# Kernel optimization log

Hardware: AMD Instinct MI355X
Metric: run time of the kernel (lower is better)

## Reference

```python
import jax, jax.numpy as jnp
import numpy as np

B, N, E = 4, 10000, 160000
D, H, HID, DE = 128, 4, 128, 16
DK = HID // H


def setup_inputs() -> dict:
    key = jax.random.key(0)
    ks = jax.random.split(key, 16)
    w = lambda k, shape: jax.random.normal(k, shape, jnp.float32) * 0.02
    return {
        "x": jax.random.normal(ks[0], (B, N, D), jnp.float32),
        "edge_index": jax.random.randint(ks[1], (2, E), 0, N, dtype=jnp.int32),
        "edge_attr": jax.random.normal(ks[2], (E, DE), jnp.float32),
        "Wq": w(ks[3], (D, HID)), "bq": jnp.zeros((HID,), jnp.float32),
        "Wk": w(ks[4], (D, HID)), "bk": jnp.zeros((HID,), jnp.float32),
        "Wv": w(ks[5], (D, HID)), "bv": jnp.zeros((HID,), jnp.float32),
        "Wf": w(ks[6], (DE, 2 * HID)), "bf": jnp.zeros((2 * HID,), jnp.float32),
        "Wo": w(ks[7], (HID, D)), "bo": jnp.zeros((D,), jnp.float32),
        "ln_g": jnp.ones((D,), jnp.float32), "ln_b": jnp.zeros((D,), jnp.float32),
    }


def reference(x, edge_index, edge_attr, Wq, bq, Wk, bk, Wv, bv, Wf, bf, Wo, bo, ln_g, ln_b):
    src, dst = edge_index[0], edge_index[1]
    # node projections -> [B, N, H, DK]
    Q = (x @ Wq + bq).reshape(B, N, H, DK)
    K = (x @ Wk + bk).reshape(B, N, H, DK)
    V = (x @ Wv + bv).reshape(B, N, H, DK)
    # edge gathers -> [B, E, H, DK]
    q_e, k_e, v_e = Q[:, dst], K[:, src], V[:, src]
    # FiLM modulation of keys (edge-conditioned, shared across batch)
    gamma, beta = jnp.split(edge_attr @ Wf + bf, 2, axis=-1)
    gamma = gamma.reshape(1, E, H, DK)
    beta = beta.reshape(1, E, H, DK)
    k_e = k_e * (1.0 + gamma) + beta
    logits = (q_e * k_e).sum(-1) / np.sqrt(DK).astype(np.float32)  # [B, E, H]

    def seg_softmax(lg):  # lg: [E, H], softmax over edges sharing a dst node
        m = jax.ops.segment_max(lg, dst, num_segments=N)       # [N, H]
        ex = jnp.exp(lg - m[dst])
        s = jax.ops.segment_sum(ex, dst, num_segments=N)        # [N, H]
        return ex / s[dst]

    att = jax.vmap(seg_softmax)(logits)                         # [B, E, H]
    msg = att[..., None] * v_e                                  # [B, E, H, DK]
    agg = jax.vmap(lambda m: jax.ops.segment_sum(m, dst, num_segments=N))(msg)
    y = agg.reshape(B, N, HID) @ Wo + bo                        # [B, N, D]
    h = x + y  # dropout is identity in eval mode
    mu = h.mean(-1, keepdims=True)
    var = ((h - mu) ** 2).mean(-1, keepdims=True)
    return (h - mu) / jnp.sqrt(var + 1e-5) * ln_g + ln_b
```

## Files before the change

### kernel.cpp

```cpp
#include <hip/hip_runtime.h>
#include <hip/hip_bf16.h>

#define B_ 4
#define N_ 10000
#define E_ 160000
#define D_ 128
#define H_ 4
#define HID_ 128
#define DK_ 32
#define DE_ 16
#define PGRID 2048
#define QKV_BLKS 625
#define FILM_BLKS 512
#define HIST_BLKS 625

typedef __attribute__((ext_vector_type(8))) short short8v;
typedef __attribute__((ext_vector_type(4))) short short4v;
typedef __attribute__((ext_vector_type(4))) float f32x4;
typedef __attribute__((ext_vector_type(2))) float f32x2;

__device__ __forceinline__ short bfb(float f) {
  union { float f; unsigned u; } c; c.f = f;
  unsigned u = c.u + 0x7FFFu + ((c.u >> 16) & 1u);
  return (short)(u >> 16);
}
__device__ __forceinline__ float b2f(unsigned short u) {
  union { unsigned u; float f; } c; c.u = ((unsigned)u) << 16;
  return c.f;
}

__device__ __forceinline__ unsigned char f2fp8(float f) {
  int r = __builtin_amdgcn_cvt_pk_fp8_f32(f, f, 0, false);
  return (unsigned char)(r & 0xff);
}
__device__ __forceinline__ f32x2 fp8lo(unsigned u) {
  return __builtin_amdgcn_cvt_pk_f32_fp8((int)u, false);
}
__device__ __forceinline__ f32x2 fp8hi(unsigned u) {
  return __builtin_amdgcn_cvt_pk_f32_fp8((int)u, true);
}

__global__ __launch_bounds__(256) void wt_prep(
    const float* __restrict__ Wq, const float* __restrict__ Wk,
    const float* __restrict__ Wv, const float* __restrict__ Wo,
    short* __restrict__ wt) {
  const float* Ws[4] = {Wq, Wk, Wv, Wo};
  const int i = blockIdx.x * 256 + threadIdx.x;
  const int m = i >> 14;
  const int k = (i >> 7) & 127;
  const int n = i & 127;
  wt[(size_t)m * 16384 + n * 128 + k] = bfb(Ws[m][k * 128 + n]);
}

__global__ __launch_bounds__(256) void phase1(
    const float* __restrict__ x, const short* __restrict__ wt,
    const float* __restrict__ bq, const float* __restrict__ bk,
    const float* __restrict__ bv,
    unsigned short* __restrict__ Qb, unsigned char* __restrict__ kv8,
    const float* __restrict__ ea, const float* __restrict__ Wf,
    const float* __restrict__ bf, unsigned char* __restrict__ film8,
    const int* __restrict__ ei, int* __restrict__ cnt) {
  const int blk = blockIdx.x;

  if (blk < QKV_BLKS) {
    __shared__ short xs[4][16][136];
    const int wave = threadIdx.x >> 6;
    const int lane = threadIdx.x & 63;
    const int ln15 = lane & 15;
    const int g    = lane >> 4;
    const long rowBase = ((long)blk * 4 + wave) * 16;

    for (int i = lane; i < 16 * 32; i += 64) {
      const int r  = i >> 5;
      const int c4 = (i & 31) * 4;
      const float4 v = *(const float4*)(x + (rowBase + r) * 128 + c4);
      short4v sv; sv.x = bfb(v.x); sv.y = bfb(v.y); sv.z = bfb(v.z); sv.w = bfb(v.w);
      *(short4v*)&xs[wave][r][c4] = sv;
    }
    __syncthreads();

    short8v af[4];
#pragma unroll
    for (int kk = 0; kk < 4; ++kk)
      af[kk] = *(const short8v*)&xs[wave][ln15][kk * 32 + g * 8];

    const float* bs[3] = {bq, bk, bv};

    int bbv[4], nnv[4];
#pragma unroll
    for (int r = 0; r < 4; ++r) {
      const long row = rowBase + g * 4 + r;
      bbv[r] = (int)(row / N_);
      nnv[r] = (int)(row - (long)bbv[r] * N_);
    }

#pragma unroll
    for (int m = 0; m < 3; ++m) {
      const short* Wt = wt + (size_t)m * 16384;
      f32x4 acc[8];
#pragma unroll
      for (int cb = 0; cb < 8; ++cb) acc[cb] = (f32x4){0.f, 0.f, 0.f, 0.f};

#pragma unroll
      for (int kk = 0; kk < 4; ++kk) {
#pragma unroll
        for (int cb = 0; cb < 8; ++cb) {
          const short8v bfr =
              *(const short8v*)(Wt + (cb * 16 + ln15) * 128 + kk * 32 + g * 8);
          acc[cb] = __builtin_amdgcn_mfma_f32_16x16x32_bf16(af[kk], bfr, acc[cb], 0, 0, 0);
        }
      }

      const float* bias = bs[m];
#pragma unroll
      for (int cb = 0; cb < 8; ++cb) {
        const int col = cb * 16 + ln15;
        const float bv_ = bias[col];
#pragma unroll
        for (int r = 0; r < 4; ++r) {
          const float val = acc[cb][r] + bv_;
          if (m == 0) {
            const long row = rowBase + g * 4 + r;
            Qb[row * 128 + col] = (unsigned short)bfb(val);
          } else {
            kv8[(((size_t)nnv[r] * 4 + bbv[r]) << 8) + (m - 1) * 128 + col] = f2fp8(val);
          }
        }
      }
    }
  } else if (blk < QKV_BLKS + FILM_BLKS) {
    const int fb   = blk - QKV_BLKS;
    const int lane = threadIdx.x & 63;
    const int wave = threadIdx.x >> 6;
    const int c0 = lane * 4;

    float4 w[16];
#pragma unroll
    for (int j = 0; j < 16; ++j) w[j] = *(const float4*)(Wf + j * 256 + c0);
    const float4 bias = *(const float4*)(bf + c0);

    for (int i = fb * 4 + wave; i < E_; i += FILM_BLKS * 4) {
      const float* ep = ea + (size_t)i * 16;
      const float4 a0 = *(const float4*)ep;
      const float4 a1 = *(const float4*)(ep + 4);
      const float4 a2 = *(const float4*)(ep + 8);
      const float4 a3 = *(const float4*)(ep + 12);
      const float ev[16] = {a0.x,a0.y,a0.z,a0.w, a1.x,a1.y,a1.z,a1.w,
                            a2.x,a2.y,a2.z,a2.w, a3.x,a3.y,a3.z,a3.w};
      float ox = bias.x, oy = bias.y, oz = bias.z, ow = bias.w;
#pragma unroll
      for (int j = 0; j < 16; ++j) {
        ox = fmaf(ev[j], w[j].x, ox);
        oy = fmaf(ev[j], w[j].y, oy);
        oz = fmaf(ev[j], w[j].z, oz);
        ow = fmaf(ev[j], w[j].w, ow);
      }
      int r = __builtin_amdgcn_cvt_pk_fp8_f32(ox, oy, 0, false);
      r = __builtin_amdgcn_cvt_pk_fp8_f32(oz, ow, r, true);
      ((int*)(film8 + (size_t)i * 256))[lane] = r;
    }
  } else {
    const int e = (blk - QKV_BLKS - FILM_BLKS) * 256 + threadIdx.x;
    if (e < E_) atomicAdd(&cnt[ei[E_ + e]], 1);
  }
}

__global__ __launch_bounds__(1024) void csr_scan(const int* __restrict__ cnt,
                                                 int* __restrict__ rowptr,
                                                 int* __restrict__ fill) {
  __shared__ int part[1024];
  const int t = threadIdx.x;
  int local[10];
  int sum = 0;
#pragma unroll
  for (int i = 0; i < 10; ++i) {
    const int idx = t * 10 + i;
    local[i] = sum;
    sum += (idx < N_) ? cnt[idx] : 0;
  }
  part[t] = sum;
  __syncthreads();
  for (int off = 1; off < 1024; off <<= 1) {
    const int v = (t >= off) ? part[t - off] : 0;
    __syncthreads();
    part[t] += v;
    __syncthreads();
  }
  const int excl = (t == 0) ? 0 : part[t - 1];
#pragma unroll
  for (int i = 0; i < 10; ++i) {
    const int idx = t * 10 + i;
    if (idx <= N_) {
      const int o = excl + local[i];
      rowptr[idx] = o;
      if (idx < N_) fill[idx] = o;
    }
  }
}

__global__ __launch_bounds__(256) void csr_scatter(
    const int* __restrict__ ei, int* __restrict__ fill,
    int* __restrict__ esrc, int* __restrict__ eord) {
  const int e = blockIdx.x * 256 + threadIdx.x;
  if (e < E_) {
    const int dst = ei[E_ + e];
    const int pos = atomicAdd(&fill[dst], 1);
    esrc[pos] = ei[e];
    eord[pos] = e;
  }
}

__global__ __launch_bounds__(256) void fused_attn(
    const int* __restrict__ rowptr, const int* __restrict__ esrc,
    const int* __restrict__ eord, const unsigned char* __restrict__ film8,
    const unsigned short* __restrict__ Qb,
    const unsigned char* __restrict__ kv8, float* __restrict__ agg) {
  const int wave = threadIdx.x >> 6;
  const int lane = threadIdx.x & 63;
  const int e2 = lane >> 5;
  const int dh = (lane >> 4) & 1;
  const int b  = (lane >> 2) & 3;
  const int h  = lane & 3;
  const int col0 = h * 32 + dh * 16;

  for (int node = blockIdx.x * 4 + wave; node < N_; node += PGRID * 4) {
    const int beg = rowptr[node], end = rowptr[node + 1];

    float q[16];
    {
      const unsigned short* qp = Qb + ((size_t)b * N_ + node) * 128 + col0;
      const short8v t0 = *(const short8v*)qp;
      const short8v t1 = *(const short8v*)(qp + 8);
#pragma unroll
      for (int j = 0; j < 8; ++j) {
        q[j]     = b2f((unsigned short)t0[j]);
        q[8 + j] = b2f((unsigned short)t1[j]);
      }
    }
    float acc[16];
#pragma unroll
    for (int d = 0; d < 16; ++d) acc[d] = 0.f;
    float se = 0.f;

    for (int i0 = beg; i0 < end; i0 += 2) {
      const int ii = i0 + e2;
      const bool valid = ii < end;
      const int ic = valid ? ii : i0;
      const int src = esrc[ic];
      const int de  = eord[ic];
      const unsigned char* kp = kv8 + ((((size_t)src << 2) + b) << 8) + col0;
      const unsigned char* fp = film8 + (size_t)de * 256 + col0;
      const uint4 kw = *(const uint4*)kp;
      const uint4 vw = *(const uint4*)(kp + 128);
      const uint4 gw = *(const uint4*)fp;
      const uint4 tw = *(const uint4*)(fp + 128);
      const unsigned ks[4] = {kw.x, kw.y, kw.z, kw.w};
      const unsigned vs[4] = {vw.x, vw.y, vw.z, vw.w};
      const unsigned gs[4] = {gw.x, gw.y, gw.z, gw.w};
      const unsigned ts[4] = {tw.x, tw.y, tw.z, tw.w};

      float pacc[4] = {0.f, 0.f, 0.f, 0.f};
#pragma unroll
      for (int w = 0; w < 4; ++w) {
        const f32x2 k0 = fp8lo(ks[w]), k1 = fp8hi(ks[w]);
        const f32x2 g0 = fp8lo(gs[w]), g1 = fp8hi(gs[w]);
        const f32x2 t0 = fp8lo(ts[w]), t1 = fp8hi(ts[w]);
        float km;
        km = k0.x + fmaf(k0.x, g0.x, t0.x); pacc[w] = fmaf(q[4*w+0], km, pacc[w]);
        km = k0.y + fmaf(k0.y, g0.y, t0.y); pacc[w] = fmaf(q[4*w+1], km, pacc[w]);
        km = k1.x + fmaf(k1.x, g1.x, t1.x); pacc[w] = fmaf(q[4*w+2], km, pacc[w]);
        km = k1.y + fmaf(k1.y, g1.y, t1.y); pacc[w] = fmaf(q[4*w+3], km, pacc[w]);
      }
      float pl = (pacc[0] + pacc[1]) + (pacc[2] + pacc[3]);
      pl += __shfl_xor(pl, 16);

      float ex = __expf(pl * 0.17677669529663687f);
      ex = valid ? ex : 0.f;
      se += ex;
#pragma unroll
      for (int w = 0; w < 4; ++w) {
        const f32x2 v0 = fp8lo(vs[w]), v1 = fp8hi(vs[w]);
        acc[4*w+0] = fmaf(ex, v0.x, acc[4*w+0]);
        acc[4*w+1] = fmaf(ex, v0.y, acc[4*w+1]);
        acc[4*w+2] = fmaf(ex, v1.x, acc[4*w+2]);
        acc[4*w+3] = fmaf(ex, v1.y, acc[4*w+3]);
      }
    }

#pragma unroll
    for (int d = 0; d < 16; ++d) acc[d] += __shfl_xor(acc[d], 32);
    se += __shfl_xor(se, 32);

    if (e2 == 0) {
      const float inv = (end > beg) ? 1.f / se : 0.f;
      float* ap = agg + ((size_t)b * N_ + node) * 128 + col0;
#pragma unroll
      for (int c = 0; c < 4; ++c) {
        float4 o;
        o.x = acc[c*4+0] * inv; o.y = acc[c*4+1] * inv;
        o.z = acc[c*4+2] * inv; o.w = acc[c*4+3] * inv;
        *(float4*)(ap + c * 4) = o;
      }
    }
  }
}

__global__ __launch_bounds__(64) void out_ln_mfma(
    const float* __restrict__ agg, const short* __restrict__ wto,
    const float* __restrict__ bo, const float* __restrict__ x,
    const float* __restrict__ lng, const float* __restrict__ lnb,
    float* __restrict__ out) {
  __shared__ short as_[16][136];
  const int lane = threadIdx.x;
  const int ln15 = lane & 15;
  const int g    = lane >> 4;
  const long rowBase = (long)blockIdx.x * 16;

  for (int i = lane; i < 16 * 32; i += 64) {
    const int r  = i >> 5;
    const int c4 = (i & 31) * 4;
    const float4 v = *(const float4*)(agg + (rowBase + r) * 128 + c4);
    short4v sv; sv.x = bfb(v.x); sv.y = bfb(v.y); sv.z = bfb(v.z); sv.w = bfb(v.w);
    *(short4v*)&as_[r][c4] = sv;
  }
  __syncthreads();

  short8v af[4];
#pragma unroll
  for (int kk = 0; kk < 4; ++kk)
    af[kk] = *(const short8v*)&as_[ln15][kk * 32 + g * 8];

  f32x4 acc[8];
#pragma unroll
  for (int cb = 0; cb < 8; ++cb) acc[cb] = (f32x4){0.f, 0.f, 0.f, 0.f};

#pragma unroll
  for (int kk = 0; kk < 4; ++kk) {
#pragma unroll
    for (int cb = 0; cb < 8; ++cb) {
      const short8v bfr =
          *(const short8v*)(wto + (cb * 16 + ln15) * 128 + kk * 32 + g * 8);
      acc[cb] = __builtin_amdgcn_mfma_f32_16x16x32_bf16(af[kk], bfr, acc[cb], 0, 0, 0);
    }
  }

#pragma unroll
  for (int cb = 0; cb < 8; ++cb) {
    const int col = cb * 16 + ln15;
    const float bov = bo[col];
#pragma unroll
    for (int r = 0; r < 4; ++r) {
      const long row = rowBase + g * 4 + r;
      acc[cb][r] += bov + x[row * 128 + col];
    }
  }

  float s1[4], s2[4];
#pragma unroll
  for (int r = 0; r < 4; ++r) {
    s1[r] = 0.f; s2[r] = 0.f;
#pragma unroll
    for (int cb = 0; cb < 8; ++cb) {
      s1[r] += acc[cb][r];
      s2[r] = fmaf(acc[cb][r], acc[cb][r], s2[r]);
    }
  }
#pragma unroll
  for (int m = 1; m < 16; m <<= 1) {
#pragma unroll
    for (int r = 0; r < 4; ++r) {
      s1[r] += __shfl_xor(s1[r], m);
      s2[r] += __shfl_xor(s2[r], m);
    }
  }
  float mu[4], inv[4];
#pragma unroll
  for (int r = 0; r < 4; ++r) {
    mu[r] = s1[r] * (1.f / 128.f);
    const float var = s2[r] * (1.f / 128.f) - mu[r] * mu[r];
    inv[r] = rsqrtf(var + 1e-5f);
  }

#pragma unroll
  for (int cb = 0; cb < 8; ++cb) {
    const int col = cb * 16 + ln15;
    const float gv = lng[col], bv_ = lnb[col];
#pragma unroll
    for (int r = 0; r < 4; ++r) {
      const long row = rowBase + g * 4 + r;
      out[row * 128 + col] = (acc[cb][r] - mu[r]) * inv[r] * gv + bv_;
    }
  }
}

extern "C" void kernel_launch(void* const* d_in, const int* in_sizes, int n_in,
                              void* d_out, int out_size, void* d_ws, size_t ws_size,
                              hipStream_t stream) {
  const float* x   = (const float*)d_in[0];
  const int*   ei  = (const int*)d_in[1];
  const float* ea  = (const float*)d_in[2];
  const float* Wq  = (const float*)d_in[3];
  const float* bq  = (const float*)d_in[4];
  const float* Wk  = (const float*)d_in[5];
  const float* bk  = (const float*)d_in[6];
  const float* Wv  = (const float*)d_in[7];
  const float* bv  = (const float*)d_in[8];
  const float* Wf  = (const float*)d_in[9];
  const float* bf  = (const float*)d_in[10];
  const float* Wo  = (const float*)d_in[11];
  const float* bo  = (const float*)d_in[12];
  const float* lng = (const float*)d_in[13];
  const float* lnb = (const float*)d_in[14];
  float* out = (float*)d_out;

  const size_t NQ = (size_t)B_ * N_ * HID_;

  char* base = (char*)d_ws;
  size_t off = 0;
  unsigned short* Qb = (unsigned short*)(base + off); off += NQ * 2;
  float* agg  = (float*)(base + off); off += NQ * 4;
  unsigned char* kv8 = (unsigned char*)(base + off);
  off += (size_t)B_ * N_ * 256;
  unsigned char* film8 = (unsigned char*)(base + off);
  off += (size_t)E_ * 256;
  short* wt   = (short*)(base + off); off += 4 * 16384 * 2;
  int*  cnt    = (int*)(base + off); off += N_ * 4;
  int*  rowptr = (int*)(base + off); off += (N_ + 1) * 4;
  int*  fill   = (int*)(base + off); off += N_ * 4;
  int*  esrc   = (int*)(base + off); off += E_ * 4;
  int*  eord   = (int*)(base + off); off += E_ * 4;

  hipMemsetAsync(cnt, 0, N_ * sizeof(int), stream);

  wt_prep<<<256, 256, 0, stream>>>(Wq, Wk, Wv, Wo, wt);
  phase1<<<QKV_BLKS + FILM_BLKS + HIST_BLKS, 256, 0, stream>>>(
      x, wt, bq, bk, bv, Qb, kv8, ea, Wf, bf, film8, ei, cnt);
  csr_scan<<<1, 1024, 0, stream>>>(cnt, rowptr, fill);
  csr_scatter<<<(E_ + 255) / 256, 256, 0, stream>>>(ei, fill, esrc, eord);
  fused_attn<<<PGRID, 256, 0, stream>>>(rowptr, esrc, eord, film8, Qb, kv8, agg);
  out_ln_mfma<<<(B_ * N_) / 16, 64, 0, stream>>>(agg, wt + 3 * 16384, bo, x, lng, lnb, out);
}
```

Before: 173.4 us.

## Use MFMA for FiLM projection and vectorize QKV epilogue stores

Replaces the scalar FMA FiLM edge projection with bf16 MFMA tiles over 16 edges per wave, using a new padded bf16 transposed Wf buffer prepared in wt_prep, and doubles the number of FiLM blocks. The QKV output column mapping is permuted so each lane owns 8 contiguous columns, which lets Q be written as short8 stores and K/V as packed 8-byte fp8 stores instead of single-element scattered stores. The goal is to cut ALU work and narrow store transactions in phase1, at the cost of bf16 rounding of edge_attr and Wf before the fp8 output.

```diff
diff --git a/kernel.cpp b/kernel.cpp
--- a/kernel.cpp
+++ b/kernel.cpp
@@ -11,7 +11,7 @@
 #define DE_ 16
 #define PGRID 2048
 #define QKV_BLKS 625
-#define FILM_BLKS 512
+#define FILM_BLKS 1024
 #define HIST_BLKS 625
 
 typedef __attribute__((ext_vector_type(8))) short short8v;
@@ -28,28 +28,37 @@
   union { unsigned u; float f; } c; c.u = ((unsigned)u) << 16;
   return c.f;
 }
-
-__device__ __forceinline__ unsigned char f2fp8(float f) {
-  int r = __builtin_amdgcn_cvt_pk_fp8_f32(f, f, 0, false);
-  return (unsigned char)(r & 0xff);
-}
 __device__ __forceinline__ f32x2 fp8lo(unsigned u) {
   return __builtin_amdgcn_cvt_pk_f32_fp8((int)u, false);
 }
 __device__ __forceinline__ f32x2 fp8hi(unsigned u) {
   return __builtin_amdgcn_cvt_pk_f32_fp8((int)u, true);
+}
+__device__ __forceinline__ int pk4fp8(float a, float b, float c, float d) {
+  int r = __builtin_amdgcn_cvt_pk_fp8_f32(a, b, 0, false);
+  r = __builtin_amdgcn_cvt_pk_fp8_f32(c, d, r, true);
+  return r;
 }
 
 __global__ __launch_bounds__(256) void wt_prep(
     const float* __restrict__ Wq, const float* __restrict__ Wk,
     const float* __restrict__ Wv, const float* __restrict__ Wo,
-    short* __restrict__ wt) {
-  const float* Ws[4] = {Wq, Wk, Wv, Wo};
-  const int i = blockIdx.x * 256 + threadIdx.x;
-  const int m = i >> 14;
-  const int k = (i >> 7) & 127;
-  const int n = i & 127;
-  wt[(size_t)m * 16384 + n * 128 + k] = bfb(Ws[m][k * 128 + n]);
+    const float* __restrict__ Wf,
+    short* __restrict__ wt, short* __restrict__ wfb) {
+  const int blk = blockIdx.x;
+  if (blk < 256) {
+    const float* Ws[4] = {Wq, Wk, Wv, Wo};
+    const int i = blk * 256 + threadIdx.x;
+    const int m = i >> 14;
+    const int k = (i >> 7) & 127;
+    const int n = i & 127;
+    wt[(size_t)m * 16384 + n * 128 + k] = bfb(Ws[m][k * 128 + n]);
+  } else {
+    const int i = (blk - 256) * 256 + threadIdx.x;
+    const int col = i >> 5;
+    const int k = i & 31;
+    wfb[col * 32 + k] = (k < DE_) ? bfb(Wf[k * 256 + col]) : (short)0;
+  }
 }
 
 __global__ __launch_bounds__(256) void phase1(
@@ -57,7 +66,7 @@
     const float* __restrict__ bq, const float* __restrict__ bk,
     const float* __restrict__ bv,
     unsigned short* __restrict__ Qb, unsigned char* __restrict__ kv8,
-    const float* __restrict__ ea, const float* __restrict__ Wf,
+    const float* __restrict__ ea, const short* __restrict__ wfb,
     const float* __restrict__ bf, unsigned char* __restrict__ film8,
     const int* __restrict__ ei, int* __restrict__ cnt) {
   const int blk = blockIdx.x;
@@ -86,12 +95,12 @@
 
     const float* bs[3] = {bq, bk, bv};
 
-    int bbv[4], nnv[4];
+    int bbv4[4], nnv[4];
 #pragma unroll
     for (int r = 0; r < 4; ++r) {
       const long row = rowBase + g * 4 + r;
-      bbv[r] = (int)(row / N_);
-      nnv[r] = (int)(row - (long)bbv[r] * N_);
+      bbv4[r] = (int)(row / N_);
+      nnv[r] = (int)(row - (long)bbv4[r] * N_);
     }
 
 #pragma unroll
@@ -106,58 +115,84 @@
 #pragma unroll
         for (int cb = 0; cb < 8; ++cb) {
           const short8v bfr =
-              *(const short8v*)(Wt + (cb * 16 + ln15) * 128 + kk * 32 + g * 8);
+              *(const short8v*)(Wt + (ln15 * 8 + cb) * 128 + kk * 32 + g * 8);
           acc[cb] = __builtin_amdgcn_mfma_f32_16x16x32_bf16(af[kk], bfr, acc[cb], 0, 0, 0);
         }
       }
 
       const float* bias = bs[m];
-#pragma unroll
-      for (int cb = 0; cb < 8; ++cb) {
-        const int col = cb * 16 + ln15;
-        const float bv_ = bias[col];
+      float bvv[8];
+#pragma unroll
+      for (int cb = 0; cb < 8; ++cb) bvv[cb] = bias[ln15 * 8 + cb];
+
+#pragma unroll
+      for (int r = 0; r < 4; ++r) {
+        if (m == 0) {
+          const long row = rowBase + g * 4 + r;
+          short8v qs;
+#pragma unroll
+          for (int cb = 0; cb < 8; ++cb) qs[cb] = bfb(acc[cb][r] + bvv[cb]);
+          *(short8v*)(Qb + row * 128 + ln15 * 8) = qs;
+        } else {
+          const int d0 = pk4fp8(acc[0][r] + bvv[0], acc[1][r] + bvv[1],
+                                acc[2][r] + bvv[2], acc[3][r] + bvv[3]);
+          const int d1 = pk4fp8(acc[4][r] + bvv[4], acc[5][r] + bvv[5],
+                                acc[6][r] + bvv[6], acc[7][r] + bvv[7]);
+          uint2 st; st.x = (unsigned)d0; st.y = (unsigned)d1;
+          *(uint2*)(kv8 + (((size_t)nnv[r] * 4 + bbv4[r]) << 8) + (m - 1) * 128 +
+                    ln15 * 8) = st;
+        }
+      }
+    }
+  } else if (blk < QKV_BLKS + FILM_BLKS) {
+    const int fb_  = blk - QKV_BLKS;
+    const int wave = threadIdx.x >> 6;
+    const int lane = threadIdx.x & 63;
+    const int ln15 = lane & 15;
+    const int g    = lane >> 4;
+
+    short8v wf[16];
+#pragma unroll
+    for (int cb = 0; cb < 16; ++cb)
+      wf[cb] = *(const short8v*)(wfb + (ln15 * 16 + cb) * 32 + g * 8);
+    float fbias[16];
+#pragma unroll
+    for (int cb = 0; cb < 16; ++cb) fbias[cb] = bf[ln15 * 16 + cb];
+
+    for (int tile = fb_ * 4 + wave; tile < E_ / 16; tile += FILM_BLKS * 4) {
+      const int e0 = tile * 16;
+      short8v af = {0, 0, 0, 0, 0, 0, 0, 0};
+      if (g < 2) {
+        const float* ap = ea + (size_t)(e0 + ln15) * 16 + g * 8;
+        const float4 a0 = *(const float4*)ap;
+        const float4 a1 = *(const float4*)(ap + 4);
+        af[0] = bfb(a0.x); af[1] = bfb(a0.y); af[2] = bfb(a0.z); af[3] = bfb(a0.w);
+        af[4] = bfb(a1.x); af[5] = bfb(a1.y); af[6] = bfb(a1.z); af[7] = bfb(a1.w);
+      }
+
+#pragma unroll
+      for (int half = 0; half < 2; ++half) {
+        f32x4 acc[8];
+#pragma unroll
+        for (int c8 = 0; c8 < 8; ++c8) {
+          acc[c8] = (f32x4){0.f, 0.f, 0.f, 0.f};
+          acc[c8] = __builtin_amdgcn_mfma_f32_16x16x32_bf16(af, wf[half * 8 + c8],
+                                                            acc[c8], 0, 0, 0);
+        }
 #pragma unroll
         for (int r = 0; r < 4; ++r) {
-          const float val = acc[cb][r] + bv_;
-          if (m == 0) {
-            const long row = rowBase + g * 4 + r;
-            Qb[row * 128 + col] = (unsigned short)bfb(val);
-          } else {
-            kv8[(((size_t)nnv[r] * 4 + bbv[r]) << 8) + (m - 1) * 128 + col] = f2fp8(val);
-          }
+          const int d0 = pk4fp8(acc[0][r] + fbias[half * 8 + 0],
+                                acc[1][r] + fbias[half * 8 + 1],
+                                acc[2][r] + fbias[half * 8 + 2],
+                                acc[3][r] + fbias[half * 8 + 3]);
+          const int d1 = pk4fp8(acc[4][r] + fbias[half * 8 + 4],
+                                acc[5][r] + fbias[half * 8 + 5],
+                                acc[6][r] + fbias[half * 8 + 6],
+                                acc[7][r] + fbias[half * 8 + 7]);
+          uint2 st; st.x = (unsigned)d0; st.y = (unsigned)d1;
+          *(uint2*)(film8 + (size_t)(e0 + 4 * g + r) * 256 + ln15 * 16 + half * 8) = st;
         }
       }
-    }
-  } else if (blk < QKV_BLKS + FILM_BLKS) {
-    const int fb   = blk - QKV_BLKS;
-    const int lane = threadIdx.x & 63;
-    const int wave = threadIdx.x >> 6;
-    const int c0 = lane * 4;
-
-    float4 w[16];
-#pragma unroll
-    for (int j = 0; j < 16; ++j) w[j] = *(const float4*)(Wf + j * 256 + c0);
-    const float4 bias = *(const float4*)(bf + c0);
-
-    for (int i = fb * 4 + wave; i < E_; i += FILM_BLKS * 4) {
-      const float* ep = ea + (size_t)i * 16;
-      const float4 a0 = *(const float4*)ep;
-      const float4 a1 = *(const float4*)(ep + 4);
-      const float4 a2 = *(const float4*)(ep + 8);
-      const float4 a3 = *(const float4*)(ep + 12);
-      const float ev[16] = {a0.x,a0.y,a0.z,a0.w, a1.x,a1.y,a1.z,a1.w,
-                            a2.x,a2.y,a2.z,a2.w, a3.x,a3.y,a3.z,a3.w};
-      float ox = bias.x, oy = bias.y, oz = bias.z, ow = bias.w;
-#pragma unroll
-      for (int j = 0; j < 16; ++j) {
-        ox = fmaf(ev[j], w[j].x, ox);
-        oy = fmaf(ev[j], w[j].y, oy);
-        oz = fmaf(ev[j], w[j].z, oz);
-        ow = fmaf(ev[j], w[j].w, ow);
-      }
-      int r = __builtin_amdgcn_cvt_pk_fp8_f32(ox, oy, 0, false);
-      r = __builtin_amdgcn_cvt_pk_fp8_f32(oz, ow, r, true);
-      ((int*)(film8 + (size_t)i * 256))[lane] = r;
     }
   } else {
     const int e = (blk - QKV_BLKS - FILM_BLKS) * 256 + threadIdx.x;
@@ -424,6 +459,7 @@
   unsigned char* film8 = (unsigned char*)(base + off);
   off += (size_t)E_ * 256;
   short* wt   = (short*)(base + off); off += 4 * 16384 * 2;
+  short* wfb  = (short*)(base + off); off += 256 * 32 * 2;
   int*  cnt    = (int*)(base + off); off += N_ * 4;
   int*  rowptr = (int*)(base + off); off += (N_ + 1) * 4;
   int*  fill   = (int*)(base + off); off += N_ * 4;
@@ -432,9 +468,9 @@
 
   hipMemsetAsync(cnt, 0, N_ * sizeof(int), stream);
 
-  wt_prep<<<256, 256, 0, stream>>>(Wq, Wk, Wv, Wo, wt);
+  wt_prep<<<288, 256, 0, stream>>>(Wq, Wk, Wv, Wo, Wf, wt, wfb);
   phase1<<<QKV_BLKS + FILM_BLKS + HIST_BLKS, 256, 0, stream>>>(
-      x, wt, bq, bk, bv, Qb, kv8, ea, Wf, bf, film8, ei, cnt);
+      x, wt, bq, bk, bv, Qb, kv8, ea, wfb, bf, film8, ei, cnt);
   csr_scan<<<1, 1024, 0, stream>>>(cnt, rowptr, fill);
   csr_scatter<<<(E_ + 255) / 256, 256, 0, stream>>>(ei, fill, esrc, eord);
   fused_attn<<<PGRID, 256, 0, stream>>>(rowptr, esrc, eord, film8, Qb, kv8, agg);
```

After: 159.1 us. 8.3% less time.
